# Optimization experiments

Hardware: AMD Instinct MI355X
Metric: run time of the kernel (lower is better)

## Reference

```python
import jax, jax.numpy as jnp
import numpy as np

D_ORIENT = 12  # number of orientation slices pooled per output channel


def setup_inputs() -> dict:
    key = jax.random.key(0)
    B, C, H, W = 8, 64, 128, 128
    x = jax.random.normal(key, (B, D_ORIENT * C, H, W), dtype=jnp.float32)
    return {"x": x}


def reference(x):
    # x: [B, 12*C, H, W]. For each output channel c, find the orientation d in
    # [0, 12) whose HxW slice contains the global max of the 12 slices, then
    # output that entire HxW slice. Matches torch max_pool3d(kernel=[12,H,W])
    # followed by the index-based slice gather in the original module.
    B, C12, H, W = x.shape
    C = C12 // D_ORIENT
    xr = x.reshape(B, C, D_ORIENT, H, W)            # [B, C, 12, H, W]
    flat = xr.reshape(B, C, D_ORIENT * H * W)
    idx = jnp.argmax(flat, axis=-1)                  # [B, C] flat argmax over (12,H,W)
    d = idx // (H * W)                               # winning orientation per (b, c)
    out = jnp.take_along_axis(xr, d[:, :, None, None, None], axis=2)
    return out[:, :, 0]                              # [B, C, H, W]
```

## Files before the change

kernel.cpp:

```cpp
#include <hip/hip_runtime.h>

#define D_ORIENT 12
#define HW 16384
#define SLICE (D_ORIENT * HW)
#define NTHREADS 1024

__global__ __launch_bounds__(NTHREADS) void opool_kernel(const float* __restrict__ x,
                                                         float* __restrict__ out) {
    const int bc = blockIdx.x;
    const float* __restrict__ src = x + (size_t)bc * SLICE;
    const int tid = threadIdx.x;

    float best = -__builtin_inff();
    int bestIdx = 0;

    const float4* __restrict__ src4 = (const float4*)src;
    #pragma unroll 4
    for (int i = tid; i < SLICE / 4; i += NTHREADS) {
        float4 v = src4[i];
        int base = i * 4;
        if (v.x > best) { best = v.x; bestIdx = base; }
        if (v.y > best) { best = v.y; bestIdx = base + 1; }
        if (v.z > best) { best = v.z; bestIdx = base + 2; }
        if (v.w > best) { best = v.w; bestIdx = base + 3; }
    }

    for (int off = 32; off >= 1; off >>= 1) {
        float ov = __shfl_down(best, off, 64);
        int   oi = __shfl_down(bestIdx, off, 64);
        if (ov > best || (ov == best && oi < bestIdx)) { best = ov; bestIdx = oi; }
    }

    __shared__ float s_val[NTHREADS / 64];
    __shared__ int   s_idx[NTHREADS / 64];
    __shared__ int   s_d;
    const int wave = tid >> 6;
    const int lane = tid & 63;
    if (lane == 0) { s_val[wave] = best; s_idx[wave] = bestIdx; }
    __syncthreads();
    if (tid == 0) {
        float bv = s_val[0];
        int   bi = s_idx[0];
        #pragma unroll
        for (int w = 1; w < NTHREADS / 64; ++w) {
            float v = s_val[w];
            int   i2 = s_idx[w];
            if (v > bv || (v == bv && i2 < bi)) { bv = v; bi = i2; }
        }
        s_d = bi / HW;
    }
    __syncthreads();

    const float4* __restrict__ win = (const float4*)(src + (size_t)s_d * HW);
    float4* __restrict__ dst = (float4*)(out + (size_t)bc * HW);
    #pragma unroll
    for (int i = tid; i < HW / 4; i += NTHREADS) {
        dst[i] = win[i];
    }
}

extern "C" void kernel_launch(void* const* d_in, const int* in_sizes, int n_in,
                              void* d_out, int out_size, void* d_ws, size_t ws_size,
                              hipStream_t stream) {
    const float* x = (const float*)d_in[0];
    float* out = (float*)d_out;
    const int n_bc = out_size / HW;
    opool_kernel<<<n_bc, NTHREADS, 0, stream>>>(x, out);
}
```

Measured before the change: 516.2 us.

## Split into per-slice max kernel and separate gather kernel for more parallelism

Replaces the single kernel, which used one 1024-thread block per (b,c) pair, with two kernels. The first computes a per-slice max using 12x more blocks of 256 threads, and the second picks the winning orientation and copies that slice. The argmax index tracking becomes plain fmax, with ties resolved by lowest slice. This targets the poor occupancy of only 512 large blocks streaming 768KB each. In exchange it adds a second launch, a workspace round trip, and a reread of the winning slice, which is likely no longer cached.

```diff
diff --git a/kernel.cpp b/kernel.cpp
--- a/kernel.cpp
+++ b/kernel.cpp
@@ -2,61 +2,63 @@
 
 #define D_ORIENT 12
 #define HW 16384
-#define SLICE (D_ORIENT * HW)
-#define NTHREADS 1024
+#define NT 256
 
-__global__ __launch_bounds__(NTHREADS) void opool_kernel(const float* __restrict__ x,
-                                                         float* __restrict__ out) {
-    const int bc = blockIdx.x;
-    const float* __restrict__ src = x + (size_t)bc * SLICE;
+__global__ __launch_bounds__(NT) void slice_max_kernel(const float* __restrict__ x,
+                                                       float* __restrict__ smax) {
+    const int s = blockIdx.x;
+    const float4* __restrict__ src4 = (const float4*)(x + (size_t)s * HW);
     const int tid = threadIdx.x;
 
     float best = -__builtin_inff();
-    int bestIdx = 0;
-
-    const float4* __restrict__ src4 = (const float4*)src;
-    #pragma unroll 4
-    for (int i = tid; i < SLICE / 4; i += NTHREADS) {
-        float4 v = src4[i];
-        int base = i * 4;
-        if (v.x > best) { best = v.x; bestIdx = base; }
-        if (v.y > best) { best = v.y; bestIdx = base + 1; }
-        if (v.z > best) { best = v.z; bestIdx = base + 2; }
-        if (v.w > best) { best = v.w; bestIdx = base + 3; }
+    #pragma unroll
+    for (int i = 0; i < HW / 4 / NT; ++i) {
+        float4 v = src4[tid + i * NT];
+        float m01 = fmaxf(v.x, v.y);
+        float m23 = fmaxf(v.z, v.w);
+        best = fmaxf(best, fmaxf(m01, m23));
     }
 
-    for (int off = 32; off >= 1; off >>= 1) {
-        float ov = __shfl_down(best, off, 64);
-        int   oi = __shfl_down(bestIdx, off, 64);
-        if (ov > best || (ov == best && oi < bestIdx)) { best = ov; bestIdx = oi; }
-    }
+    #pragma unroll
+    for (int off = 32; off >= 1; off >>= 1)
+        best = fmaxf(best, __shfl_down(best, off, 64));
 
-    __shared__ float s_val[NTHREADS / 64];
-    __shared__ int   s_idx[NTHREADS / 64];
-    __shared__ int   s_d;
+    __shared__ float s_w[NT / 64];
     const int wave = tid >> 6;
     const int lane = tid & 63;
-    if (lane == 0) { s_val[wave] = best; s_idx[wave] = bestIdx; }
+    if (lane == 0) s_w[wave] = best;
     __syncthreads();
     if (tid == 0) {
-        float bv = s_val[0];
-        int   bi = s_idx[0];
+        float m = fmaxf(fmaxf(s_w[0], s_w[1]), fmaxf(s_w[2], s_w[3]));
+        smax[s] = m;
+    }
+}
+
+__global__ __launch_bounds__(NT) void gather_kernel(const float* __restrict__ x,
+                                                    const float* __restrict__ smax,
+                                                    float* __restrict__ out) {
+    const int bc = blockIdx.x;
+    __shared__ int s_d;
+    if (threadIdx.x == 0) {
+        const float* __restrict__ m = smax + bc * D_ORIENT;
+        float g = m[0];
+        int d = 0;
         #pragma unroll
-        for (int w = 1; w < NTHREADS / 64; ++w) {
-            float v = s_val[w];
-            int   i2 = s_idx[w];
-            if (v > bv || (v == bv && i2 < bi)) { bv = v; bi = i2; }
+        for (int k = 1; k < D_ORIENT; ++k) {
+            float v = m[k];
+            if (v > g) { g = v; d = k; }
         }
-        s_d = bi / HW;
+        s_d = d;
     }
     __syncthreads();
 
-    const float4* __restrict__ win = (const float4*)(src + (size_t)s_d * HW);
+    const float4* __restrict__ win =
+        (const float4*)(x + ((size_t)bc * D_ORIENT + (size_t)s_d) * HW);
     float4* __restrict__ dst = (float4*)(out + (size_t)bc * HW);
+    const int tid = threadIdx.x;
     #pragma unroll
-    for (int i = tid; i < HW / 4; i += NTHREADS) {
-        dst[i] = win[i];
-    }
+    for (int i = 0; i < HW / 4 / NT; ++i)
+        dst[tid + i * NT] = win[tid + i * NT];
 }
 
 extern "C" void kernel_launch(void* const* d_in, const int* in_sizes, int n_in,
@@ -64,6 +66,9 @@
                               hipStream_t stream) {
     const float* x = (const float*)d_in[0];
     float* out = (float*)d_out;
+    float* smax = (float*)d_ws;
     const int n_bc = out_size / HW;
-    opool_kernel<<<n_bc, NTHREADS, 0, stream>>>(x, out);
+
+    slice_max_kernel<<<n_bc * D_ORIENT, NT, 0, stream>>>(x, smax);
+    gather_kernel<<<n_bc, NT, 0, stream>>>(x, smax, out);
 }
```

New measurement: 531.1 us. 2.9% more time.
